# Kernel optimization log

Hardware: AMD Instinct MI355X
Metric: run time of the kernel (lower is better)

Reference implementation:

```python
import jax, jax.numpy as jnp
import numpy as np

R_EARTH_KM = 6371.0

def haversine(lat1, lon1, lat2, lon2):
    # inputs in degrees, output distance in km
    lat1, lon1, lat2, lon2 = (jnp.radians(x) for x in (lat1, lon1, lat2, lon2))
    dlat = lat2 - lat1
    dlon = lon2 - lon1
    a = jnp.sin(dlat * 0.5) ** 2 + jnp.cos(lat1) * jnp.cos(lat2) * jnp.sin(dlon * 0.5) ** 2
    return 2.0 * R_EARTH_KM * jnp.arcsin(jnp.sqrt(jnp.clip(a, 0.0, 1.0)))

def _latlon(key, n):
    k1, k2 = jax.random.split(key)
    lat = jax.random.uniform(k1, (n,), minval=-90.0, maxval=90.0)
    lon = jax.random.uniform(k2, (n,), minval=-180.0, maxval=180.0)
    return jnp.stack([lat, lon], axis=1).astype(jnp.float32)

def setup_inputs() -> dict:
    key = jax.random.key(0)
    ks = jax.random.split(key, 12)
    B, D = 4096, 1792
    NC, NM, NF = 3000, 7000, 13000
    scale = 0.02
    return {
        'features': jax.random.normal(ks[0], (B, D), dtype=jnp.float32),
        'labels_2d': _latlon(ks[1], B),
        'coarse_partition': _latlon(ks[2], NC),
        'middle_partition': _latlon(ks[3], NM),
        'fine_partition': _latlon(ks[4], NF),
        'middle_parents': jax.random.randint(ks[5], (NM,), 0, NC, dtype=jnp.int32),
        'fine_parents': jax.random.randint(ks[6], (NF,), 0, NM, dtype=jnp.int32),
        'coarse_w': jax.random.normal(ks[7], (D, NC), dtype=jnp.float32) * scale,
        'coarse_b': jnp.zeros((NC,), dtype=jnp.float32),
        'middle_w': jax.random.normal(ks[8], (D, NM), dtype=jnp.float32) * scale,
        'middle_b': jnp.zeros((NM,), dtype=jnp.float32),
        'fine_w': jax.random.normal(ks[9], (D, NF), dtype=jnp.float32) * scale,
        'fine_b': jnp.zeros((NF,), dtype=jnp.float32),
    }

def _single_loss(labels_2d, logits, partition):
    # cartesian-product haversine cdist: [B, M]
    dists = haversine(labels_2d[:, 0:1], labels_2d[:, 1:2],
                      partition[None, :, 0], partition[None, :, 1])
    labels_index = jnp.argmin(dists, axis=1)
    logp = jax.nn.log_softmax(logits, axis=1)
    nll = -jnp.take_along_axis(logp, labels_index[:, None], axis=1)[:, 0]
    return jnp.mean(nll)

def reference(features, labels_2d, coarse_partition, middle_partition, fine_partition,
              middle_parents, fine_parents, coarse_w, coarse_b, middle_w, middle_b,
              fine_w, fine_b):
    coarse_logits = features @ coarse_w + coarse_b
    middle_logits = features @ middle_w + middle_b
    fine_logits = features @ fine_w + fine_b

    loss = (_single_loss(labels_2d, coarse_logits, coarse_partition)
            + _single_loss(labels_2d, middle_logits, middle_partition)
            + _single_loss(labels_2d, fine_logits, fine_partition))

    fine_probs = jax.nn.softmax(fine_logits, axis=1)
    middle_probs = jax.nn.softmax(middle_logits, axis=1)
    coarse_probs = jax.nn.softmax(coarse_logits, axis=1)
    # hierarchy combine: gather parent probs and multiply
    final_probs = (fine_probs
                   * middle_probs[:, fine_parents]
                   * coarse_probs[:, middle_parents[fine_parents]])

    predictions = fine_partition[jnp.argmax(final_probs, axis=1)]  # [B, 2]
    d = haversine(labels_2d[:, 0], labels_2d[:, 1], predictions[:, 0], predictions[:, 1])
    thresholds = jnp.array([1.0, 25.0, 200.0, 750.0, 2500.0], dtype=jnp.float32)
    acc = jnp.mean((d[None, :] <= thresholds[:, None]).astype(jnp.float32), axis=1)
    return loss, acc
```

## Files before the change

### kernel.cpp

```cpp
#include <hip/hip_runtime.h>
#include <hip/hip_fp16.h>
#include <math.h>

#define B_   4096
#define D_   1792
#define NC_  3000
#define NM_  7000
#define NF_  13000
#define NCP  3072
#define NMP  7168
#define NFP  13312
#define NTOT (NCP + NMP + NFP)
#define OFFC 0
#define OFFM NCP
#define OFFF (NCP + NMP)
#define FHALF 6656
#define WCHUNK 7168
#define NIT 14
#define DEG2RAD 0.017453292519943295f

typedef _Float16 half8  __attribute__((ext_vector_type(8)));
typedef _Float16 half4v __attribute__((ext_vector_type(4)));
typedef float    f32x4  __attribute__((ext_vector_type(4)));

__device__ __forceinline__ void async16(const void* g, void* l) {
  __builtin_amdgcn_global_load_lds(
      (const __attribute__((address_space(1))) void*)g,
      (__attribute__((address_space(3))) void*)l, 16, 0, 0);
}

__global__ void prep_kernel(const float* __restrict__ labels,
                            const float* __restrict__ cp, const float* __restrict__ mp,
                            const float* __restrict__ fp,
                            const float* __restrict__ cb, const float* __restrict__ mb,
                            const float* __restrict__ fb,
                            float* __restrict__ bias, float4* __restrict__ ptrig,
                            float4* __restrict__ ltrig, float* __restrict__ accum) {
  int i = blockIdx.x * 256 + threadIdx.x;
  if (i < NTOT) {
    float v = 0.f;
    if (i < OFFM)      { if (i < NC_) v = cb[i]; }
    else if (i < OFFF) { int j = i - OFFM; if (j < NM_) v = mb[j]; }
    else               { int j = i - OFFF; if (j < NF_) v = fb[j]; }
    bias[i] = v;
  }
  if (i < NC_ + NM_ + NF_) {
    const float* src; int j = i;
    if (i < NC_)            { src = cp; }
    else if (i < NC_ + NM_) { src = mp; j = i - NC_; }
    else                    { src = fp; j = i - NC_ - NM_; }
    float la = src[2 * j] * DEG2RAD, lo = src[2 * j + 1] * DEG2RAD;
    float sla, cla, slo, clo;
    sincosf(la, &sla, &cla); sincosf(lo, &slo, &clo);
    ptrig[i] = make_float4(sla, cla, slo, clo);
  }
  if (i < B_) {
    float la = labels[2 * i] * DEG2RAD, lo = labels[2 * i + 1] * DEG2RAD;
    float sla, cla, slo, clo;
    sincosf(la, &sla, &cla); sincosf(lo, &slo, &clo);
    ltrig[i] = make_float4(sla, cla, slo, clo);
  }
  if (i < 64) accum[i] = 0.f;
}

__global__ void cvt_feat(const float4* __restrict__ in, half4v* __restrict__ out) {
  int i = blockIdx.x * 256 + threadIdx.x;
  float4 v = in[i];
  half4v h;
  h[0] = (_Float16)v.x; h[1] = (_Float16)v.y; h[2] = (_Float16)v.z; h[3] = (_Float16)v.w;
  out[i] = h;
}

__global__ void transpose_w(const float* __restrict__ w, _Float16* __restrict__ wt,
                            int Nfull, int c0, int ntrue_chunk) {
  __shared__ float tile[32][33];
  int n0 = blockIdx.x * 32, k0 = blockIdx.y * 32;
  int tx = threadIdx.x, ty = threadIdx.y;
#pragma unroll
  for (int i = 0; i < 4; ++i) {
    int kk = ty + i * 8;
    int n = n0 + tx;
    float v = (n < ntrue_chunk) ? w[(size_t)(k0 + kk) * Nfull + c0 + n] : 0.f;
    tile[kk][tx] = v;
  }
  __syncthreads();
#pragma unroll
  for (int i = 0; i < 4; ++i) {
    int nn = ty + i * 8;
    wt[(size_t)(n0 + nn) * D_ + k0 + tx] = (_Float16)tile[tx][nn];
  }
}

__global__ void argmin_kernel(const float4* __restrict__ ptrig, const float4* __restrict__ ltrig,
                              int* __restrict__ lidx) {
  __shared__ float rv[256];
  __shared__ int ri[256];
  int b = blockIdx.x, tid = threadIdx.x;
  float4 lt = ltrig[b];
  const int base[3] = {0, NC_, NC_ + NM_};
  const int cnt[3]  = {NC_, NM_, NF_};
#pragma unroll
  for (int h = 0; h < 3; ++h) {
    float best = 1e30f; int bi = 0;
    for (int i = tid; i < cnt[h]; i += 256) {
      float4 pt = ptrig[base[h] + i];
      float cdla = lt.y * pt.y + lt.x * pt.x;
      float cdlo = lt.w * pt.w + lt.z * pt.z;
      float a = 0.5f * (1.f - cdla) + (lt.y * pt.y) * 0.5f * (1.f - cdlo);
      if (a < best) { best = a; bi = i; }
    }
    rv[tid] = best; ri[tid] = bi;
    __syncthreads();
    for (int o = 128; o; o >>= 1) {
      if (tid < o) {
        if (rv[tid + o] < rv[tid] || (rv[tid + o] == rv[tid] && ri[tid + o] < ri[tid])) {
          rv[tid] = rv[tid + o]; ri[tid] = ri[tid + o];
        }
      }
      __syncthreads();
    }
    if (tid == 0) lidx[h * B_ + b] = ri[0];
    __syncthreads();
  }
}

#define LOADA(abase) { _Pragma("unroll") for (int tm = 0; tm < 8; ++tm) \
    af[tm] = *(const half8*)(lds + (abase) + amB + tm * 512 + xsl); }
#define LOADB(bbase, tn) (*(const half8*)(lds + (bbase) + bnB + (tn) * 512 + xsl))
#define DO_MFMA(nh) { \
    __builtin_amdgcn_s_setprio(1); \
    _Pragma("unroll") for (int tm = 0; tm < 8; ++tm) { \
      acc[tm][(nh)*2]   = __builtin_amdgcn_mfma_f32_16x16x32_f16(af[tm], b0, acc[tm][(nh)*2], 0,0,0); \
      acc[tm][(nh)*2+1] = __builtin_amdgcn_mfma_f32_16x16x32_f16(af[tm], b1, acc[tm][(nh)*2+1], 0,0,0); \
    } \
    __builtin_amdgcn_s_setprio(0); }

__global__ __launch_bounds__(512, 2) void gemm_f16(const _Float16* __restrict__ A,
                                                   const _Float16* __restrict__ Bt,
                                                   const float* __restrict__ bias,
                                                   _Float16* __restrict__ C, int coff) {
  __shared__ _Float16 lds[65536];
  const int tid = threadIdx.x;
  const int lane = tid & 63, w = tid >> 6;
  const int wm = w & 1, wn = w >> 1;
  const int q = lane >> 4, l15 = lane & 15;
  const int bx = blockIdx.x;
  const int mt = bx & 15, nt = bx >> 4;
  const int m0 = mt * 256;
  const int nl0 = nt * 256;
  const int gn0 = coff + nl0;

  f32x4 acc[8][4];
#pragma unroll
  for (int a = 0; a < 8; ++a)
#pragma unroll
    for (int b2 = 0; b2 < 4; ++b2) acc[a][b2] = (f32x4){0.f, 0.f, 0.f, 0.f};

  const int amB = (wm * 128 + l15) * 32;
  const int bnB = (wn * 64 + l15) * 32;
  const int xsl = ((q ^ ((l15 >> 1) & 3)) << 3);
  const int kbl = (lane & 3) ^ ((lane >> 3) & 3);
  const int rr = lane >> 2;

  auto stage = [&](const _Float16* __restrict__ G, int row0, int ktile, int kh, int ldsoff) {
    const int kk = ktile * 64 + (kh * 4 + kbl) * 8;
#pragma unroll
    for (int j = 0; j < 2; ++j) {
      int seg = w * 2 + j;
      async16(G + (size_t)(row0 + seg * 16 + rr) * D_ + kk,
              (void*)(lds + ldsoff + seg * 512));
    }
  };

  half8 af[8];

  stage(A,  m0,  0, 0, 0);
  stage(Bt, nl0, 0, 0, 32768);
  stage(A,  m0,  0, 1, 8192);
  stage(Bt, nl0, 0, 1, 40960);
  stage(A,  m0,  1, 0, 16384);
  stage(Bt, nl0, 1, 0, 49152);
  asm volatile("s_waitcnt vmcnt(4)" ::: "memory");
  __builtin_amdgcn_sched_barrier(0);
  __builtin_amdgcn_s_barrier();

#pragma unroll 1
  for (int i = 0; i < NIT; ++i) {
    const int t1 = 2 * i + 1, t2 = 2 * i + 2, t3 = 2 * i + 3;
    const bool more = (i < NIT - 1);
    LOADA(0);
    { half8 b0 = LOADB(32768, 0), b1 = LOADB(32768, 1);
      stage(A,  m0,  t1, 1, 24576);
      stage(Bt, nl0, t1, 1, 57344);
      __builtin_amdgcn_s_barrier();
      DO_MFMA(0);
      __builtin_amdgcn_s_barrier(); }
    { half8 b0 = LOADB(32768, 2), b1 = LOADB(32768, 3);
      __builtin_amdgcn_s_barrier();
      DO_MFMA(1);
      __builtin_amdgcn_s_barrier(); }
    LOADA(8192);
    { half8 b0 = LOADB(40960, 0), b1 = LOADB(40960, 1);
      if (more) stage(A, m0, t2, 0, 0);
      __builtin_amdgcn_s_barrier();
      DO_MFMA(0);
      __builtin_amdgcn_s_barrier(); }
    { half8 b0 = LOADB(40960, 2), b1 = LOADB(40960, 3);
      if (more) {
        stage(Bt, nl0, t2, 0, 32768);
        asm volatile("s_waitcnt vmcnt(4)" ::: "memory");
      } else {
        asm volatile("s_waitcnt vmcnt(0)" ::: "memory");
      }
      __builtin_amdgcn_sched_barrier(0);
      __builtin_amdgcn_s_barrier();
      DO_MFMA(1);
      __builtin_amdgcn_s_barrier(); }
    LOADA(16384);
    { half8 b0 = LOADB(49152, 0), b1 = LOADB(49152, 1);
      if (more) { stage(A, m0, t2, 1, 8192); stage(Bt, nl0, t2, 1, 40960); }
      __builtin_amdgcn_s_barrier();
      DO_MFMA(0);
      __builtin_amdgcn_s_barrier(); }
    { half8 b0 = LOADB(49152, 2), b1 = LOADB(49152, 3);
      __builtin_amdgcn_s_barrier();
      DO_MFMA(1);
      __builtin_amdgcn_s_barrier(); }
    LOADA(24576);
    { half8 b0 = LOADB(57344, 0), b1 = LOADB(57344, 1);
      if (more) stage(A, m0, t3, 0, 16384);
      __builtin_amdgcn_s_barrier();
      DO_MFMA(0);
      __builtin_amdgcn_s_barrier(); }
    { half8 b0 = LOADB(57344, 2), b1 = LOADB(57344, 3);
      if (more) stage(Bt, nl0, t3, 0, 49152);
      asm volatile("s_waitcnt vmcnt(4)" ::: "memory");
      __builtin_amdgcn_sched_barrier(0);
      __builtin_amdgcn_s_barrier();
      DO_MFMA(1);
      __builtin_amdgcn_s_barrier(); }
  }

  float bn[4];
#pragma unroll
  for (int tn = 0; tn < 4; ++tn) bn[tn] = bias[gn0 + wn * 64 + tn * 16 + l15];
#pragma unroll
  for (int tm = 0; tm < 8; ++tm) {
    int gm = m0 + wm * 128 + tm * 16 + q * 4;
#pragma unroll
    for (int tn = 0; tn < 4; ++tn) {
      int gn = gn0 + wn * 64 + tn * 16 + l15;
      _Float16* dst = C + (size_t)gm * NTOT + gn;
#pragma unroll
      for (int r = 0; r < 4; ++r) dst[(size_t)r * NTOT] = (_Float16)(acc[tm][tn][r] + bn[tn]);
    }
  }
}

__device__ __forceinline__ float block_lse(float m, float s, float* ms, float* ss, int tid) {
  ms[tid] = m; ss[tid] = s;
  __syncthreads();
  for (int o = 128; o; o >>= 1) {
    if (tid < o) {
      float m2 = ms[tid + o], s2 = ss[tid + o];
      if (m2 > ms[tid]) { ss[tid] = s2 + ss[tid] * __expf(ms[tid] - m2); ms[tid] = m2; }
      else ss[tid] += s2 * __expf(m2 - ms[tid]);
    }
    __syncthreads();
  }
  float r = ms[0] + logf(ss[0]);
  __syncthreads();
  return r;
}

__global__ __launch_bounds__(256) void final_kernel(const _Float16* __restrict__ logits,
                                                    const int* __restrict__ mpar,
                                                    const int* __restrict__ fpar,
                                                    const float4* __restrict__ ptrig,
                                                    const float4* __restrict__ ltrig,
                                                    const int* __restrict__ lidx,
                                                    float* __restrict__ nll_buf,
                                                    float* __restrict__ accum) {
  __shared__ float co[NC_];
  __shared__ float par[NM_];
  __shared__ float ms[256], ss[256];
  __shared__ int ri[256];
  int b = blockIdx.x, tid = threadIdx.x;
  const _Float16* row = logits + (size_t)b * NTOT;

  float m = -1e30f, s = 0.f;
  {
    const half8* rc = (const half8*)(row + OFFC);
    for (int i = tid; i < NC_ / 8; i += 256) {
      half8 v = rc[i];
      float x[8];
#pragma unroll
      for (int j = 0; j < 8; ++j) x[j] = (float)v[j];
      float vm = fmaxf(fmaxf(fmaxf(x[0], x[1]), fmaxf(x[2], x[3])),
                       fmaxf(fmaxf(x[4], x[5]), fmaxf(x[6], x[7])));
      if (vm > m) { s *= __expf(m - vm); m = vm; }
#pragma unroll
      for (int j = 0; j < 8; ++j) s += __expf(x[j] - m);
      f32x4 lo = {x[0], x[1], x[2], x[3]}, hi = {x[4], x[5], x[6], x[7]};
      *(f32x4*)(co + i * 8)     = lo;
      *(f32x4*)(co + i * 8 + 4) = hi;
    }
  }
  float lseC = block_lse(m, s, ms, ss, tid);

  m = -1e30f; s = 0.f;
  {
    const half8* rm = (const half8*)(row + OFFM);
    const int4* mp4 = (const int4*)mpar;
    for (int i = tid; i < NM_ / 8; i += 256) {
      half8 v = rm[i];
      int4 p0 = mp4[2 * i], p1 = mp4[2 * i + 1];
      float x[8];
#pragma unroll
      for (int j = 0; j < 8; ++j) x[j] = (float)v[j];
      float vm = fmaxf(fmaxf(fmaxf(x[0], x[1]), fmaxf(x[2], x[3])),
                       fmaxf(fmaxf(x[4], x[5]), fmaxf(x[6], x[7])));
      if (vm > m) { s *= __expf(m - vm); m = vm; }
#pragma unroll
      for (int j = 0; j < 8; ++j) s += __expf(x[j] - m);
      int pj[8] = {p0.x, p0.y, p0.z, p0.w, p1.x, p1.y, p1.z, p1.w};
      f32x4 lo = {x[0] + co[pj[0]], x[1] + co[pj[1]], x[2] + co[pj[2]], x[3] + co[pj[3]]};
      f32x4 hi = {x[4] + co[pj[4]], x[5] + co[pj[5]], x[6] + co[pj[6]], x[7] + co[pj[7]]};
      *(f32x4*)(par + i * 8)     = lo;
      *(f32x4*)(par + i * 8 + 4) = hi;
    }
  }
  float lseM = block_lse(m, s, ms, ss, tid);

  m = -1e30f; s = 0.f;
  float best = -1e30f; int bi = 0;
  {
    const half8* rf = (const half8*)(row + OFFF);
    const int4* fp4 = (const int4*)fpar;
    for (int i = tid; i < NF_ / 8; i += 256) {
      half8 v = rf[i];
      int4 p0 = fp4[2 * i], p1 = fp4[2 * i + 1];
      float x[8];
#pragma unroll
      for (int j = 0; j < 8; ++j) x[j] = (float)v[j];
      float vm = fmaxf(fmaxf(fmaxf(x[0], x[1]), fmaxf(x[2], x[3])),
                       fmaxf(fmaxf(x[4], x[5]), fmaxf(x[6], x[7])));
      if (vm > m) { s *= __expf(m - vm); m = vm; }
#pragma unroll
      for (int j = 0; j < 8; ++j) s += __expf(x[j] - m);
      int pj[8] = {p0.x, p0.y, p0.z, p0.w, p1.x, p1.y, p1.z, p1.w};
#pragma unroll
      for (int j = 0; j < 8; ++j) {
        float vv = x[j] + par[pj[j]];
        if (vv > best) { best = vv; bi = i * 8 + j; }
      }
    }
  }
  float lseF = block_lse(m, s, ms, ss, tid);

  ms[tid] = best; ri[tid] = bi;
  __syncthreads();
  for (int o = 128; o; o >>= 1) {
    if (tid < o) {
      if (ms[tid + o] > ms[tid] || (ms[tid + o] == ms[tid] && ri[tid + o] < ri[tid])) {
        ms[tid] = ms[tid + o]; ri[tid] = ri[tid + o];
      }
    }
    __syncthreads();
  }

  if (tid == 0) {
    int ic = lidx[b], im = lidx[B_ + b], ifn = lidx[2 * B_ + b];
    nll_buf[b] = (lseC - (float)row[OFFC + ic])
               + (lseM - (float)row[OFFM + im])
               + (lseF - (float)row[OFFF + ifn]);
    float4 pt = ptrig[NC_ + NM_ + ri[0]];
    float4 lt = ltrig[b];
    float cdla = lt.y * pt.y + lt.x * pt.x;
    float cdlo = lt.w * pt.w + lt.z * pt.z;
    float a = 0.5f * (1.f - cdla) + (lt.y * pt.y) * 0.5f * (1.f - cdlo);
    a = fminf(fmaxf(a, 0.f), 1.f);
    float d = 2.f * 6371.f * asinf(sqrtf(a));
    const float thr[5] = {1.f, 25.f, 200.f, 750.f, 2500.f};
#pragma unroll
    for (int j = 0; j < 5; ++j)
      if (d <= thr[j]) atomicAdd(accum + 1 + j, 1.f);
  }
}

__global__ void finish_kernel(const float* __restrict__ accum,
                              const float* __restrict__ nll, float* __restrict__ out) {
  __shared__ float sh[256];
  int tid = threadIdx.x;
  float s = 0.f;
  for (int i = tid; i < B_; i += 256) s += nll[i];
  sh[tid] = s;
  __syncthreads();
  for (int o = 128; o; o >>= 1) { if (tid < o) sh[tid] += sh[tid + o]; __syncthreads(); }
  if (tid == 0) out[0] = sh[0] * (1.f / 4096.f);
  if (tid >= 1 && tid < 6) out[tid] = accum[tid] * (1.f / 4096.f);
}

extern "C" void kernel_launch(void* const* d_in, const int* in_sizes, int n_in,
                              void* d_out, int out_size, void* d_ws, size_t ws_size,
                              hipStream_t stream) {
  (void)in_sizes; (void)n_in; (void)out_size; (void)ws_size;
  const float* features = (const float*)d_in[0];
  const float* labels   = (const float*)d_in[1];
  const float* cpart    = (const float*)d_in[2];
  const float* mpart    = (const float*)d_in[3];
  const float* fpart    = (const float*)d_in[4];
  const int*   mpar     = (const int*)d_in[5];
  const int*   fpar     = (const int*)d_in[6];
  const float* cw       = (const float*)d_in[7];
  const float* cb       = (const float*)d_in[8];
  const float* mw       = (const float*)d_in[9];
  const float* mb       = (const float*)d_in[10];
  const float* fw       = (const float*)d_in[11];
  const float* fb       = (const float*)d_in[12];
  float* out = (float*)d_out;

  char* ws = (char*)d_ws;
  size_t off = 0;
  auto alloc = [&](size_t bytes) {
    char* p = ws + off;
    off += (bytes + 255) & ~(size_t)255;
    return p;
  };
  _Float16* feat16 = (_Float16*)alloc((size_t)B_ * D_ * 2);
  _Float16* wTbuf  = (_Float16*)alloc((size_t)WCHUNK * D_ * 2);
  _Float16* logits = (_Float16*)alloc((size_t)B_ * NTOT * 2);
  float*    bias   = (float*)alloc((size_t)NTOT * 4);
  float4*   ptrig  = (float4*)alloc((size_t)(NC_ + NM_ + NF_) * 16);
  float4*   ltrig  = (float4*)alloc((size_t)B_ * 16);
  int*      lidx   = (int*)alloc((size_t)3 * B_ * 4);
  float*    nll    = (float*)alloc((size_t)B_ * 4);
  float*    accum  = (float*)alloc(64 * 4);

  prep_kernel<<<dim3(NTOT / 256), dim3(256), 0, stream>>>(labels, cpart, mpart, fpart,
                                                          cb, mb, fb, bias, ptrig, ltrig, accum);
  cvt_feat<<<dim3(B_ * D_ / 4 / 256), dim3(256), 0, stream>>>((const float4*)features,
                                                              (half4v*)feat16);
  argmin_kernel<<<dim3(B_), dim3(256), 0, stream>>>(ptrig, ltrig, lidx);

  transpose_w<<<dim3(NCP / 32, D_ / 32), dim3(32, 8), 0, stream>>>(cw, wTbuf, NC_, 0, NC_);
  gemm_f16<<<dim3(16 * (NCP / 256)), dim3(512), 0, stream>>>(feat16, wTbuf, bias, logits, OFFC);

  transpose_w<<<dim3(NMP / 32, D_ / 32), dim3(32, 8), 0, stream>>>(mw, wTbuf, NM_, 0, NM_);
  gemm_f16<<<dim3(16 * (NMP / 256)), dim3(512), 0, stream>>>(feat16, wTbuf, bias, logits, OFFM);

  transpose_w<<<dim3(FHALF / 32, D_ / 32), dim3(32, 8), 0, stream>>>(fw, wTbuf, NF_, 0, FHALF);
  gemm_f16<<<dim3(16 * (FHALF / 256)), dim3(512), 0, stream>>>(feat16, wTbuf, bias, logits, OFFF);

  transpose_w<<<dim3(FHALF / 32, D_ / 32), dim3(32, 8), 0, stream>>>(fw, wTbuf, NF_, FHALF, NF_ - FHALF);
  gemm_f16<<<dim3(16 * (FHALF / 256)), dim3(512), 0, stream>>>(feat16, wTbuf, bias, logits, OFFF + FHALF);

  final_kernel<<<dim3(B_), dim3(256), 0, stream>>>(logits, mpar, fpar, ptrig, ltrig,
                                                   lidx, nll, accum);
  finish_kernel<<<dim3(1), dim3(256), 0, stream>>>(accum, nll, out);
}
```

Before: 797.0 us.

## Merge GEMM MFMA sub-phases per k-slice and remap blocks across XCDs

Each k-slice now loads all four B fragments at once and issues 32 MFMAs between a single pair of barriers, instead of two 16-MFMA sub-phases with four barriers. This halves the workgroup barriers in the main loop and gives longer uninterrupted MFMA runs. Block indices are also permuted so consecutive tiles land on the same XCD, which should improve L2 reuse of the A and B panels. The cost is two more live half8 registers for B fragments, which could affect occupancy or scheduling at 2 blocks per CU.

```diff
diff --git a/kernel.cpp b/kernel.cpp
--- a/kernel.cpp
+++ b/kernel.cpp
@@ -126,12 +126,13 @@
 
 #define LOADA(abase) { _Pragma("unroll") for (int tm = 0; tm < 8; ++tm) \
     af[tm] = *(const half8*)(lds + (abase) + amB + tm * 512 + xsl); }
-#define LOADB(bbase, tn) (*(const half8*)(lds + (bbase) + bnB + (tn) * 512 + xsl))
-#define DO_MFMA(nh) { \
+#define LOADBALL(bbase) { _Pragma("unroll") for (int tn = 0; tn < 4; ++tn) \
+    bf[tn] = *(const half8*)(lds + (bbase) + bnB + tn * 512 + xsl); }
+#define DO_MFMA32 { \
     __builtin_amdgcn_s_setprio(1); \
     _Pragma("unroll") for (int tm = 0; tm < 8; ++tm) { \
-      acc[tm][(nh)*2]   = __builtin_amdgcn_mfma_f32_16x16x32_f16(af[tm], b0, acc[tm][(nh)*2], 0,0,0); \
-      acc[tm][(nh)*2+1] = __builtin_amdgcn_mfma_f32_16x16x32_f16(af[tm], b1, acc[tm][(nh)*2+1], 0,0,0); \
+      _Pragma("unroll") for (int tn = 0; tn < 4; ++tn) \
+        acc[tm][tn] = __builtin_amdgcn_mfma_f32_16x16x32_f16(af[tm], bf[tn], acc[tm][tn], 0,0,0); \
     } \
     __builtin_amdgcn_s_setprio(0); }
 
@@ -144,7 +145,9 @@
   const int lane = tid & 63, w = tid >> 6;
   const int wm = w & 1, wn = w >> 1;
   const int q = lane >> 4, l15 = lane & 15;
-  const int bx = blockIdx.x;
+  const int nwg = gridDim.x, q8 = nwg >> 3;
+  const int bxr = blockIdx.x;
+  const int bx = (bxr & 7) * q8 + (bxr >> 3);
   const int mt = bx & 15, nt = bx >> 4;
   const int m0 = mt * 256;
   const int nl0 = nt * 256;
@@ -172,7 +175,7 @@
     }
   };
 
-  half8 af[8];
+  half8 af[8], bf[4];
 
   stage(A,  m0,  0, 0, 0);
   stage(Bt, nl0, 0, 0, 32768);
@@ -189,56 +192,45 @@
     const int t1 = 2 * i + 1, t2 = 2 * i + 2, t3 = 2 * i + 3;
     const bool more = (i < NIT - 1);
     LOADA(0);
-    { half8 b0 = LOADB(32768, 0), b1 = LOADB(32768, 1);
-      stage(A,  m0,  t1, 1, 24576);
-      stage(Bt, nl0, t1, 1, 57344);
-      __builtin_amdgcn_s_barrier();
-      DO_MFMA(0);
-      __builtin_amdgcn_s_barrier(); }
-    { half8 b0 = LOADB(32768, 2), b1 = LOADB(32768, 3);
-      __builtin_amdgcn_s_barrier();
-      DO_MFMA(1);
-      __builtin_amdgcn_s_barrier(); }
+    LOADBALL(32768);
+    stage(A,  m0,  t1, 1, 24576);
+    stage(Bt, nl0, t1, 1, 57344);
+    __builtin_amdgcn_s_barrier();
+    DO_MFMA32;
+    __builtin_amdgcn_s_barrier();
     LOADA(8192);
-    { half8 b0 = LOADB(40960, 0), b1 = LOADB(40960, 1);
-      if (more) stage(A, m0, t2, 0, 0);
-      __builtin_amdgcn_s_barrier();
-      DO_MFMA(0);
-      __builtin_amdgcn_s_barrier(); }
-    { half8 b0 = LOADB(40960, 2), b1 = LOADB(40960, 3);
-      if (more) {
-        stage(Bt, nl0, t2, 0, 32768);
-        asm volatile("s_waitcnt vmcnt(4)" ::: "memory");
-      } else {
-        asm volatile("s_waitcnt vmcnt(0)" ::: "memory");
-      }
-      __builtin_amdgcn_sched_barrier(0);
-      __builtin_amdgcn_s_barrier();
-      DO_MFMA(1);
-      __builtin_amdgcn_s_barrier(); }
+    LOADBALL(40960);
+    if (more) {
+      stage(A,  m0,  t2, 0, 0);
+      stage(Bt, nl0, t2, 0, 32768);
+      asm volatile("s_waitcnt vmcnt(4)" ::: "memory");
+    } else {
+      asm volatile("s_waitcnt vmcnt(0)" ::: "memory");
+    }
+    __builtin_amdgcn_sched_barrier(0);
+    __builtin_amdgcn_s_barrier();
+    DO_MFMA32;
+    __builtin_amdgcn_s_barrier();
     LOADA(16384);
-    { half8 b0 = LOADB(49152, 0), b1 = LOADB(49152, 1);
-      if (more) { stage(A, m0, t2, 1, 8192); stage(Bt, nl0, t2, 1, 40960); }
-      __builtin_amdgcn_s_barrier();
-      DO_MFMA(0);
-      __builtin_amdgcn_s_barrier(); }
-    { half8 b0 = LOADB(49152, 2), b1 = LOADB(49152, 3);
-      __builtin_amdgcn_s_barrier();
-      DO_MFMA(1);
-      __builtin_amdgcn_s_barrier(); }
+    LOADBALL(49152);
+    if (more) {
+      stage(A,  m0,  t2, 1, 8192);
+      stage(Bt, nl0, t2, 1, 40960);
+    }
+    __builtin_amdgcn_s_barrier();
+    DO_MFMA32;
+    __builtin_amdgcn_s_barrier();
     LOADA(24576);
-    { half8 b0 = LOADB(57344, 0), b1 = LOADB(57344, 1);
-      if (more) stage(A, m0, t3, 0, 16384);
-      __builtin_amdgcn_s_barrier();
-      DO_MFMA(0);
-      __builtin_amdgcn_s_barrier(); }
-    { half8 b0 = LOADB(57344, 2), b1 = LOADB(57344, 3);
-      if (more) stage(Bt, nl0, t3, 0, 49152);
+    LOADBALL(57344);
+    if (more) {
+      stage(A,  m0,  t3, 0, 16384);
+      stage(Bt, nl0, t3, 0, 49152);
       asm volatile("s_waitcnt vmcnt(4)" ::: "memory");
       __builtin_amdgcn_sched_barrier(0);
-      __builtin_amdgcn_s_barrier();
-      DO_MFMA(1);
-      __builtin_amdgcn_s_barrier(); }
+    }
+    __builtin_amdgcn_s_barrier();
+    DO_MFMA32;
+    __builtin_amdgcn_s_barrier();
   }
 
   float bn[4];
```

Measured after the change: 800.5 us. About the same (+0.4%).
